# Optimization experiments

Hardware: AMD Instinct MI355X
Metric: run time of the kernel (lower is better)

The kernel has to match this reference:

```python
import jax, jax.numpy as jnp
import numpy as np

NUM_FILTER = 256
CAPS_LEN = 8
NUM_EMOTIONS = 8
OUT_DIM = 16
NUM_CHANNEL = 25
TIME_LEN = 25
NUM_CAPS = NUM_CHANNEL * TIME_LEN * (NUM_FILTER // CAPS_LEN)  # 20000
NUM_ITERATIONS = 3


def setup_inputs() -> dict:
    key = jax.random.key(0)
    ks = jax.random.split(key, 10)
    B = 32
    x = jax.random.normal(ks[0], (B, 54, 54), jnp.float32)
    conv1_w = jax.random.normal(ks[1], (NUM_FILTER, 1, 6, 6), jnp.float32) * 0.05
    conv1_b = jax.random.normal(ks[2], (NUM_FILTER,), jnp.float32) * 0.01
    conv2_w = jax.random.normal(ks[3], (NUM_FILTER, NUM_FILTER, 6, 6), jnp.float32) * 0.01
    conv2_b = jax.random.normal(ks[4], (NUM_FILTER,), jnp.float32) * 0.01
    conv3_w = jax.random.normal(ks[5], (NUM_FILTER, 2 * NUM_FILTER, 1, 1), jnp.float32) * 0.05
    conv3_b = jax.random.normal(ks[6], (NUM_FILTER,), jnp.float32) * 0.01
    # PrimaryCaps: one Linear(caps_len -> caps_len) per capsule, batched as [nc, out, in]
    pc_w = jax.random.normal(ks[7], (NUM_CAPS, CAPS_LEN, CAPS_LEN), jnp.float32) * 0.1
    pc_b = jax.random.normal(ks[8], (NUM_CAPS, CAPS_LEN), jnp.float32) * 0.1
    # EmotionCaps transform W: [nc, num_emotions, out_dim, in_dim]
    W = jax.random.normal(ks[9], (NUM_CAPS, NUM_EMOTIONS, OUT_DIM, CAPS_LEN), jnp.float32) * 0.05
    return {"x": x, "conv1_w": conv1_w, "conv1_b": conv1_b, "conv2_w": conv2_w,
            "conv2_b": conv2_b, "conv3_w": conv3_w, "conv3_b": conv3_b,
            "pc_w": pc_w, "pc_b": pc_b, "W": W}


def _conv(x, w, b, stride):
    y = jax.lax.conv_general_dilated(x, w, (stride, stride), 'VALID',
                                     dimension_numbers=('NCHW', 'OIHW', 'NCHW'))
    return y + b[None, :, None, None]


def _squash(s):
    # scale = |s|^2 / (1 + |s|^2); out = scale * s / (|s| + 1e-8)
    n2 = jnp.sum(s * s, axis=-1, keepdims=True)
    n = jnp.sqrt(n2)
    return (n2 / (1.0 + n2)) * s / (n + 1e-8)


def reference(x, conv1_w, conv1_b, conv2_w, conv2_b, conv3_w, conv3_b, pc_w, pc_b, W):
    x4 = x[:, None]                                    # [B,1,54,54]
    x1 = jax.nn.relu(_conv(x4, conv1_w, conv1_b, 2))   # [B,F,25,25]
    y = jnp.pad(x1, ((0, 0), (0, 0), (2, 3), (2, 3)))  # ZeroPad2d((2,3,2,3))
    y = jax.nn.relu(_conv(y, conv2_w, conv2_b, 1))     # [B,F,25,25]
    z = jax.nn.relu(jnp.concatenate([x1, y], axis=1))  # [B,2F,25,25]
    z = _conv(z, conv3_w, conv3_b, 1)                  # [B,F,25,25]
    B, F, H, Wd = z.shape
    # flatten to capsules: [B, F//caps_len, caps_len, H*W] -> [B, nc, caps_len]
    caps = z.reshape(B, F // CAPS_LEN, CAPS_LEN, H * Wd)
    caps = caps.transpose(0, 1, 3, 2).reshape(B, NUM_CAPS, CAPS_LEN)
    # PrimaryCaps: per-capsule linear, batched as a single einsum
    u = jnp.einsum('bni,noi->bno', caps, pc_w) + pc_b[None]   # [B,nc,caps_len]
    # EmotionCaps: u_hat[b,n,e,o] = W[n,e,o,i] u[b,n,i]
    u_hat = jnp.einsum('bni,neoi->bneo', u, W)                # [B,nc,ne,out_dim]
    b = jnp.zeros((B, NUM_CAPS, NUM_EMOTIONS), u.dtype)
    v = None
    for r in range(NUM_ITERATIONS):
        c = jax.nn.softmax(b, axis=2)[..., None]              # [B,nc,ne,1]
        v = _squash(jnp.sum(c * u_hat, axis=1))               # [B,ne,out_dim]
        if r < NUM_ITERATIONS - 1:
            b = b + jnp.einsum('bneo,beo->bne', u_hat, v)
    return jnp.linalg.norm(v, axis=-1)                        # [B,ne]
```

## Files before the change

kernel.cpp:

```cpp
#include <hip/hip_runtime.h>

typedef unsigned short u16;
typedef __attribute__((ext_vector_type(8))) short bf16x8;
typedef __attribute__((ext_vector_type(4))) float floatx4;

#define NPIX 625
#define NCAPS 20000
#define K2 9216

__device__ __forceinline__ u16 f2bf(float f) {
  unsigned u = __float_as_uint(f);
  return (u16)((u + 0x7fffu + ((u >> 16) & 1u)) >> 16);
}

__device__ __forceinline__ float bf2f(unsigned v) {
  return __uint_as_float(v << 16);
}

#define GLDS16(g, l) __builtin_amdgcn_global_load_lds( \
    (const __attribute__((address_space(1))) void*)(g), \
    (__attribute__((address_space(3))) void*)(l), 16, 0, 0)

__global__ void prep_weights2(const float* __restrict__ w2, const float* __restrict__ w3,
                              u16* __restrict__ A2c, u16* __restrict__ A3) {
  if (blockIdx.x < 256) {
    const int oc = blockIdx.x, c = threadIdx.x;
    const float* src = w2 + (oc * 256 + c) * 36;
    float v[36];
#pragma unroll
    for (int k = 0; k < 9; k++) {
      const float4 q = *(const float4*)(src + k * 4);
      v[k * 4 + 0] = q.x; v[k * 4 + 1] = q.y; v[k * 4 + 2] = q.z; v[k * 4 + 3] = q.w;
    }
    const int mtile = oc >> 7, row = oc & 127;
#pragma unroll
    for (int t = 0; t < 36; t++) {
      const int kt = t / 9, tl = t % 9;
      A2c[(kt * 2 + mtile) * 294912 + row * 2304 + tl * 256 + c] = f2bf(v[t]);
    }
  } else {
    const int j = (blockIdx.x - 256) * 1024 + threadIdx.x * 4;
    const float4 q = *(const float4*)(w3 + j);
    ushort4 p;
    p.x = f2bf(q.x); p.y = f2bf(q.y); p.z = f2bf(q.z); p.w = f2bf(q.w);
    *(ushort4*)(A3 + j) = p;
  }
}

__global__ void prep_wbs(const float* __restrict__ W, u16* __restrict__ Wbs) {
  int r = blockIdx.x * 256 + threadIdx.x;
  int n = r >> 7, eo = r & 127;
  int e = eo >> 4, o = eo & 15;
  const float* src = W + n * 1024 + eo * 8;
  const float4 v0 = *(const float4*)src;
  const float4 v1 = *(const float4*)(src + 4);
  u16* dst = Wbs + n * 1088 + e * 136 + o * 8;
  ushort4 p0, p1;
  p0.x = f2bf(v0.x); p0.y = f2bf(v0.y); p0.z = f2bf(v0.z); p0.w = f2bf(v0.w);
  p1.x = f2bf(v1.x); p1.y = f2bf(v1.y); p1.z = f2bf(v1.z); p1.w = f2bf(v1.w);
  *(ushort4*)dst = p0;
  *(ushort4*)(dst + 4) = p1;
}

__global__ void conv1_kernel(const float* __restrict__ x, const float* __restrict__ w1,
                             const float* __restrict__ b1, u16* __restrict__ x1p) {
  int blk = blockIdx.x;
  int b = blk / 25, i = blk % 25;
  int f = threadIdx.x;
  float wreg[36];
#pragma unroll
  for (int k = 0; k < 36; k++) wreg[k] = w1[f * 36 + k];
  float bias = b1[f];
  const float* xb = x + b * 54 * 54 + (2 * i) * 54;
  for (int j = 0; j < 25; j++) {
    float acc = bias;
#pragma unroll
    for (int ki = 0; ki < 6; ki++)
#pragma unroll
      for (int kj = 0; kj < 6; kj++)
        acc = fmaf(xb[ki * 54 + 2 * j + kj], wreg[ki * 6 + kj], acc);
    x1p[(((b * 30 + i + 2) * 30) + (j + 2)) * 256 + f] = f2bf(fmaxf(acc, 0.f));
  }
}

__global__ __launch_bounds__(256) void conv2_gemm(const u16* __restrict__ A2c,
    const u16* __restrict__ x1p, u16* __restrict__ P) {
  __shared__ u16 As0[128 * 32];
  __shared__ u16 Bs0[128 * 32];
  __shared__ u16 As1[128 * 32];
  __shared__ u16 Bs1[128 * 32];
  const int tid = threadIdx.x;
  const int lane = tid & 63, wave = tid >> 6;
  const int f = blockIdx.x;
  const int w = (f & 7) * 157 + (f >> 3);
  const int ntile = w >> 3, combo = w & 7;
  const int kt = combo >> 1, mtile = combo & 1;
  const int t0 = kt * 9;

  const int seg0 = tid, seg1 = tid + 256;
  const u16* gA0 = A2c + combo * 294912 + (seg0 >> 2) * 2304 + (seg0 & 3) * 8;
  const u16* gA1 = A2c + combo * 294912 + (seg1 >> 2) * 2304 + (seg1 & 3) * 8;

  auto pixbase = [&](int seg) {
    int n = ntile * 128 + (seg >> 2);
    if (n > NCAPS - 1) n = NCAPS - 1;
    int b = n / NPIX, p = n % NPIX;
    int i = p / 25, j = p % 25;
    return ((b * 30 + i) * 30 + j) * 256 + (seg & 3) * 8;
  };
  const u16* gb0 = x1p + pixbase(seg0);
  const u16* gb1 = x1p + pixbase(seg1);

// ... 24 lines not shown
        bfr[tt] = *(const bf16x8*)(Bs0 + (wn * 64 + tt * 16 + lrow) * 32 + kgrp * 8);
      }
#pragma unroll
      for (int tm = 0; tm < 4; tm++)
#pragma unroll
        for (int tn = 0; tn < 4; tn++)
          acc[tm][tn] = __builtin_amdgcn_mfma_f32_16x16x32_bf16(af[tm], bfr[tn], acc[tm][tn], 0, 0, 0);
#pragma unroll
      for (int tt = 0; tt < 4; tt++) {
        af[tt]  = *(const bf16x8*)(As1 + (wm * 64 + tt * 16 + lrow) * 32 + kgrp * 8);
        bfr[tt] = *(const bf16x8*)(Bs1 + (wn * 64 + tt * 16 + lrow) * 32 + kgrp * 8);
      }
#pragma unroll
      for (int tm = 0; tm < 4; tm++)
#pragma unroll
        for (int tn = 0; tn < 4; tn++)
          acc[tm][tn] = __builtin_amdgcn_mfma_f32_16x16x32_bf16(af[tm], bfr[tn], acc[tm][tn], 0, 0, 0);
      __syncthreads();
    }
    boff += 256;
    kj++;
    if (kj == 6) { kj = 0; boff += 6144; }
  }

  u16* Pk = P + kt * 5120000;
  const int nb = ntile * 128 + wn * 64;
  const int ocb = mtile * 128 + wm * 64 + kgrp * 4;
#pragma unroll
  for (int tn = 0; tn < 4; tn++) {
    int n = nb + tn * 16 + lrow;
    if (n < NCAPS) {
#pragma unroll
      for (int tm = 0; tm < 4; tm++) {
        int oc = ocb + tm * 16;
        ushort4 pk;
        pk.x = f2bf(acc[tm][tn][0]);
        pk.y = f2bf(acc[tm][tn][1]);
        pk.z = f2bf(acc[tm][tn][2]);
        pk.w = f2bf(acc[tm][tn][3]);
        *(ushort4*)(Pk + n * 256 + oc) = pk;
      }
    }
  }
}

__global__ void conv2_red(const u16* __restrict__ P, const float* __restrict__ bias2,
                          u16* __restrict__ y) {
  const int idx = blockIdx.x * 256 + threadIdx.x;
  const ushort4 p0 = *(const ushort4*)(P + idx * 4);
  const ushort4 p1 = *(const ushort4*)(P + 5120000 + idx * 4);
  const ushort4 p2 = *(const ushort4*)(P + 10240000 + idx * 4);
  const ushort4 p3 = *(const ushort4*)(P + 15360000 + idx * 4);
  const float4 bs = *(const float4*)(bias2 + ((idx * 4) & 255));
  float sx = bf2f(p0.x) + bf2f(p1.x) + bf2f(p2.x) + bf2f(p3.x) + bs.x;
  float sy = bf2f(p0.y) + bf2f(p1.y) + bf2f(p2.y) + bf2f(p3.y) + bs.y;
  float sz = bf2f(p0.z) + bf2f(p1.z) + bf2f(p2.z) + bf2f(p3.z) + bs.z;
  float sw = bf2f(p0.w) + bf2f(p1.w) + bf2f(p2.w) + bf2f(p3.w) + bs.w;
  ushort4 pk;
  pk.x = f2bf(fmaxf(sx, 0.f));
  pk.y = f2bf(fmaxf(sy, 0.f));
  pk.z = f2bf(fmaxf(sz, 0.f));
  pk.w = f2bf(fmaxf(sw, 0.f));
  *(ushort4*)(y + idx * 4) = pk;
}

__global__ __launch_bounds__(256) void conv3_gemm(const u16* __restrict__ A3,
    const u16* __restrict__ x1p, const u16* __restrict__ y,
    const float* __restrict__ bias3, float* __restrict__ z) {
  __shared__ u16 As[128 * 32];
  __shared__ u16 Bs[128 * 32];
  const int tid = threadIdx.x;
  const int lane = tid & 63, wave = tid >> 6;
  const int mtile = blockIdx.x, ntile = blockIdx.y;

  const int seg0 = tid, seg1 = tid + 256;
  const u16* ga0 = A3 + (mtile * 128 + (seg0 >> 2)) * 512 + (seg0 & 3) * 8;
  const u16* ga1 = A3 + (mtile * 128 + (seg1 >> 2)) * 512 + (seg1 & 3) * 8;

  auto mkbases = [&](int seg, const u16*& gx, const u16*& gy) {
    int n = ntile * 128 + (seg >> 2);
    if (n > NCAPS - 1) n = NCAPS - 1;
    int b = n / NPIX, p = n % NPIX;
    int i = p / 25, j = p % 25;
    gx = x1p + ((b * 30 + i + 2) * 30 + (j + 2)) * 256 + (seg & 3) * 8;
    gy = y + n * 256 + (seg & 3) * 8;
  };
  const u16 *gx0, *gy0, *gx1, *gy1;
  mkbases(seg0, gx0, gy0);
  mkbases(seg1, gx1, gy1);

  floatx4 acc[4][4] = {};
  const int wm = wave & 1, wn = wave >> 1;
  const int lrow = lane & 15, kgrp = lane >> 4;

  for (int kc = 0; kc < 16; kc++) {
    const u16* s0 = (kc < 8) ? (gx0 + kc * 32) : (gy0 + (kc - 8) * 32);
    const u16* s1 = (kc < 8) ? (gx1 + kc * 32) : (gy1 + (kc - 8) * 32);
    GLDS16(ga0 + kc * 32, As + seg0 * 8);
    GLDS16(ga1 + kc * 32, As + seg1 * 8);
    GLDS16(s0, Bs + seg0 * 8);
    GLDS16(s1, Bs + seg1 * 8);
    __syncthreads();
    bf16x8 af[4], bfr[4];
#pragma unroll
    for (int tt = 0; tt < 4; tt++) {
      af[tt]  = *(const bf16x8*)(As + (wm * 64 + tt * 16 + lrow) * 32 + kgrp * 8);
      bfr[tt] = *(const bf16x8*)(Bs + (wn * 64 + tt * 16 + lrow) * 32 + kgrp * 8);
    }
#pragma unroll
    for (int tm = 0; tm < 4; tm++)
#pragma unroll
      for (int tn = 0; tn < 4; tn++)
        acc[tm][tn] = __builtin_amdgcn_mfma_f32_16x16x32_bf16(af[tm], bfr[tn], acc[tm][tn], 0, 0, 0);
    __syncthreads();
  }

  const int nb = ntile * 128 + wn * 64;
  const int fb = mtile * 128 + wm * 64 + kgrp * 4;
#pragma unroll
  for (int tn = 0; tn < 4; tn++) {
    int n = nb + tn * 16 + lrow;
    if (n < NCAPS) {
#pragma unroll
      for (int tm = 0; tm < 4; tm++) {
        int f0 = fb + tm * 16;
        float4 v;
        v.x = acc[tm][tn][0] + bias3[f0 + 0];
        v.y = acc[tm][tn][1] + bias3[f0 + 1];
        v.z = acc[tm][tn][2] + bias3[f0 + 2];
        v.w = acc[tm][tn][3] + bias3[f0 + 3];
        *(float4*)(z + n * 256 + f0) = v;
      }
    }
  }
}


__device__ __forceinline__ float dot8v(float4 a0, float4 a1, float4 b0, float4 b1) {
  float s = a0.x * b0.x;
  s = fmaf(a0.y, b0.y, s); s = fmaf(a0.z, b0.z, s); s = fmaf(a0.w, b0.w, s);
  s = fmaf(a1.x, b1.x, s); s = fmaf(a1.y, b1.y, s);
  s = fmaf(a1.z, b1.z, s); s = fmaf(a1.w, b1.w, s);
  return s;
}

__device__ __forceinline__ float dotrow(uint4 w, float4 ua, float4 ub) {
  float s = __uint_as_float(w.x << 16) * ua.x;
  s = fmaf(__uint_as_float(w.x & 0xffff0000u), ua.y, s);
  s = fmaf(__uint_as_float(w.y << 16), ua.z, s);
  s = fmaf(__uint_as_float(w.y & 0xffff0000u), ua.w, s);
  s = fmaf(__uint_as_float(w.z << 16), ub.x, s);
  s = fmaf(__uint_as_float(w.z & 0xffff0000u), ub.y, s);
  s = fmaf(__uint_as_float(w.w << 16), ub.z, s);
  s = fmaf(__uint_as_float(w.w & 0xffff0000u), ub.w, s);
  return s;
}

__global__ void caps_u(const float* __restrict__ z, const float* __restrict__ pcw,
                       const float* __restrict__ pcb, float* __restrict__ u) {
  const int tid = threadIdx.x;
  const int b = tid >> 3, o = tid & 7;
  for (int k = 0; k < 8; k++) {
    const int n = blockIdx.x * 8 + k;
    const int g = n / NPIX, p = n % NPIX;
    const float* zp = z + (b * NPIX + p) * 256 + g * 8;
    float4 c0 = *(const float4*)zp;
    float4 c1 = *(const float4*)(zp + 4);
    const float* pw = pcw + n * 64 + o * 8;
    float4 w0 = *(const float4*)pw;
    float4 w1 = *(const float4*)(pw + 4);
    u[n * 256 + tid] = pcb[n * 8 + o] + dot8v(w0, w1, c0, c1);
  }
}

__global__ void caps_u2(const float* __restrict__ z, const float* __restrict__ pcw,
                        const float* __restrict__ pcb, unsigned* __restrict__ u2) {
  const int tid = threadIdx.x;
  const int b = tid >> 3, o = tid & 7;
  for (int k = 0; k < 8; k++) {
    const int n = blockIdx.x * 8 + k;
    const int g = n / NPIX, p = n % NPIX;
    const float* zp = z + (b * NPIX + p) * 256 + g * 8;
    float4 c0 = *(const float4*)zp;
    float4 c1 = *(const float4*)(zp + 4);
    const float* pw = pcw + n * 64 + o * 8;
    float4 w0 = *(const float4*)pw;
    float4 w1 = *(const float4*)(pw + 4);
    const float myu = pcb[n * 8 + o] + dot8v(w0, w1, c0, c1);
    const float partner = __shfl_xor(myu, 1, 64);
    if (!(o & 1)) {
      unsigned pk = (unsigned)f2bf(myu) | ((unsigned)f2bf(partner) << 16);
      u2[n * 128 + b * 4 + (o >> 1)] = pk;
    }
  }
}

__global__ __launch_bounds__(256, 4) void caps_accb2(const unsigned* __restrict__ u2,
    const u16* __restrict__ Wbs, const float* __restrict__ vsum,
    float* __restrict__ Spart) {
  __shared__ u16 Ws[16 * 1088];
  const int tid = threadIdx.x;
  const int b = tid >> 3, e = tid & 7;
  const int n0 = blockIdx.x * 16;

  const u16* gsrc = Wbs + n0 * 1088;
#pragma unroll
  for (int k = 0; k < 9; k++) {
    const int idx = k * 256 + tid;
    if (idx < 2176) GLDS16(gsrc + idx * 8, Ws + idx * 8);
  }

  const float* vp = vsum + tid * 16;
  const float4 V0 = *(const float4*)vp;
  const float4 V1 = *(const float4*)(vp + 4);
  const float4 V2 = *(const float4*)(vp + 8);
  const float4 V3 = *(const float4*)(vp + 12);
  float s0 = 0.f, s1 = 0.f, s2 = 0.f, s3 = 0.f, s4 = 0.f, s5 = 0.f, s6 = 0.f, s7 = 0.f;
  float s8 = 0.f, s9 = 0.f, s10 = 0.f, s11 = 0.f, s12 = 0.f, s13 = 0.f, s14 = 0.f, s15 = 0.f;

  __syncthreads();

  for (int it = 0; it < 16; it++) {
    const int n = n0 + it;
    const uint4 up = *(const uint4*)(u2 + n * 128 + b * 4);
    float4 ua, ub;
    ua.x = __uint_as_float(up.x << 16); ua.y = __uint_as_float(up.x & 0xffff0000u);
    ua.z = __uint_as_float(up.y << 16); ua.w = __uint_as_float(up.y & 0xffff0000u);
    ub.x = __uint_as_float(up.z << 16); ub.y = __uint_as_float(up.z & 0xffff0000u);
    ub.z = __uint_as_float(up.w << 16); ub.w = __uint_as_float(up.w & 0xffff0000u);

    const u16* Wn = Ws + it * 1088 + e * 136;
    float h0, h1, h2, h3, h4, h5, h6, h7, h8, h9, h10, h11, h12, h13, h14, h15;
#define ROW(o, H) { uint4 w = *(const uint4*)(Wn + (o) * 8); H = dotrow(w, ua, ub); }
    ROW(0, h0)   ROW(1, h1)   ROW(2, h2)   ROW(3, h3)
    ROW(4, h4)   ROW(5, h5)   ROW(6, h6)   ROW(7, h7)
    ROW(8, h8)   ROW(9, h9)   ROW(10, h10) ROW(11, h11)
    ROW(12, h12) ROW(13, h13) ROW(14, h14) ROW(15, h15)
#undef ROW
    float blog = h0 * V0.x;
    blog = fmaf(h1, V0.y, blog);  blog = fmaf(h2, V0.z, blog);  blog = fmaf(h3, V0.w, blog);
    blog = fmaf(h4, V1.x, blog);  blog = fmaf(h5, V1.y, blog);  blog = fmaf(h6, V1.z, blog);
    blog = fmaf(h7, V1.w, blog);  blog = fmaf(h8, V2.x, blog);  blog = fmaf(h9, V2.y, blog);
    blog = fmaf(h10, V2.z, blog); blog = fmaf(h11, V2.w, blog); blog = fmaf(h12, V3.x, blog);
    blog = fmaf(h13, V3.y, blog); blog = fmaf(h14, V3.z, blog); blog = fmaf(h15, V3.w, blog);
    float m = blog;
    m = fmaxf(m, __shfl_xor(m, 1, 64));
    m = fmaxf(m, __shfl_xor(m, 2, 64));
    m = fmaxf(m, __shfl_xor(m, 4, 64));
    float ex = __expf(blog - m);
    float ss = ex;
    ss += __shfl_xor(ss, 1, 64);
    ss += __shfl_xor(ss, 2, 64);
    ss += __shfl_xor(ss, 4, 64);
    const float c = ex / ss;
    s0 = fmaf(c, h0, s0);   s1 = fmaf(c, h1, s1);   s2 = fmaf(c, h2, s2);   s3 = fmaf(c, h3, s3);
    s4 = fmaf(c, h4, s4);   s5 = fmaf(c, h5, s5);   s6 = fmaf(c, h6, s6);   s7 = fmaf(c, h7, s7);
    s8 = fmaf(c, h8, s8);   s9 = fmaf(c, h9, s9);   s10 = fmaf(c, h10, s10); s11 = fmaf(c, h11, s11);
    s12 = fmaf(c, h12, s12); s13 = fmaf(c, h13, s13); s14 = fmaf(c, h14, s14); s15 = fmaf(c, h15, s15);
  }
  float* Sp = Spart + blockIdx.x * 4096 + tid * 16;
  *(float4*)(Sp + 0)  = make_float4(s0, s1, s2, s3);
  *(float4*)(Sp + 4)  = make_float4(s4, s5, s6, s7);
  *(float4*)(Sp + 8)  = make_float4(s8, s9, s10, s11);
  *(float4*)(Sp + 12) = make_float4(s12, s13, s14, s15);
}

__global__ __launch_bounds__(256, 2) void caps_acc(const float* __restrict__ u,
    const float* __restrict__ W, const float* __restrict__ vsum,
    float* __restrict__ Spart) {
  const int tid = threadIdx.x;
  const int b = tid >> 3, e = tid & 7;
  const float* vp = vsum + tid * 16;
  const float4 V0 = *(const float4*)vp;
  const float4 V1 = *(const float4*)(vp + 4);
  const float4 V2 = *(const float4*)(vp + 8);
  const float4 V3 = *(const float4*)(vp + 12);
  float s0 = 0.f, s1 = 0.f, s2 = 0.f, s3 = 0.f, s4 = 0.f, s5 = 0.f, s6 = 0.f, s7 = 0.f;
  float s8 = 0.f, s9 = 0.f, s10 = 0.f, s11 = 0.f, s12 = 0.f, s13 = 0.f, s14 = 0.f, s15 = 0.f;
  const int n0 = blockIdx.x * 16;
  for (int it = 0; it < 16; it++) {
    const int n = n0 + it;
    const float* un = u + n * 256 + (b << 3);
    const float4 u0 = *(const float4*)un;
    const float4 u1 = *(const float4*)(un + 4);
    const float* Wn = W + n * 1024 + e * 128;
    float h0, h1, h2, h3, h4, h5, h6, h7, h8, h9, h10, h11, h12, h13, h14, h15;
#define OST(o, H) { float4 wa = *(const float4*)(Wn + (o) * 8); \
                    float4 wb = *(const float4*)(Wn + (o) * 8 + 4); \
                    H = dot8v(wa, wb, u0, u1); }
    OST(0, h0)  OST(1, h1)  OST(2, h2)  OST(3, h3)
    OST(4, h4)  OST(5, h5)  OST(6, h6)  OST(7, h7)
    OST(8, h8)  OST(9, h9)  OST(10, h10) OST(11, h11)
    OST(12, h12) OST(13, h13) OST(14, h14) OST(15, h15)
#undef OST
    float blog = h0 * V0.x;
    blog = fmaf(h1, V0.y, blog);  blog = fmaf(h2, V0.z, blog);  blog = fmaf(h3, V0.w, blog);
    blog = fmaf(h4, V1.x, blog);  blog = fmaf(h5, V1.y, blog);  blog = fmaf(h6, V1.z, blog);
    blog = fmaf(h7, V1.w, blog);  blog = fmaf(h8, V2.x, blog);  blog = fmaf(h9, V2.y, blog);
    blog = fmaf(h10, V2.z, blog); blog = fmaf(h11, V2.w, blog); blog = fmaf(h12, V3.x, blog);
    blog = fmaf(h13, V3.y, blog); blog = fmaf(h14, V3.z, blog); blog = fmaf(h15, V3.w, blog);
    float m = blog;
    m = fmaxf(m, __shfl_xor(m, 1, 64));
    m = fmaxf(m, __shfl_xor(m, 2, 64));
    m = fmaxf(m, __shfl_xor(m, 4, 64));
    float ex = __expf(blog - m);
    float ss = ex;
    ss += __shfl_xor(ss, 1, 64);
    ss += __shfl_xor(ss, 2, 64);
    ss += __shfl_xor(ss, 4, 64);
    const float c = ex / ss;
    s0 = fmaf(c, h0, s0);   s1 = fmaf(c, h1, s1);   s2 = fmaf(c, h2, s2);   s3 = fmaf(c, h3, s3);
    s4 = fmaf(c, h4, s4);   s5 = fmaf(c, h5, s5);   s6 = fmaf(c, h6, s6);   s7 = fmaf(c, h7, s7);
    s8 = fmaf(c, h8, s8);   s9 = fmaf(c, h9, s9);   s10 = fmaf(c, h10, s10); s11 = fmaf(c, h11, s11);
    s12 = fmaf(c, h12, s12); s13 = fmaf(c, h13, s13); s14 = fmaf(c, h14, s14); s15 = fmaf(c, h15, s15);
  }
  float* Sp = Spart + blockIdx.x * 4096 + tid * 16;
  *(float4*)(Sp + 0)  = make_float4(s0, s1, s2, s3);
  *(float4*)(Sp + 4)  = make_float4(s4, s5, s6, s7);
  *(float4*)(Sp + 8)  = make_float4(s8, s9, s10, s11);
  *(float4*)(Sp + 12) = make_float4(s12, s13, s14, s15);
}

__global__ void caps_redB(const float* __restrict__ Spart, float* __restrict__ Sp2) {
  const int j = blockIdx.x * 256 + threadIdx.x;
  const int r0 = blockIdx.y * 50;
  float a0 = 0.f, a1 = 0.f;
  for (int r = 0; r < 50; r += 2) {
    a0 += Spart[(r0 + r) * 4096 + j];
    a1 += Spart[(r0 + r + 1) * 4096 + j];
  }
  Sp2[blockIdx.y * 4096 + j] = a0 + a1;
}

__global__ void caps_v2(const float* __restrict__ Sp2, float* __restrict__ vsum, int add) {
  const int t = threadIdx.x;
  float4 a0 = make_float4(0.f, 0.f, 0.f, 0.f), a1 = a0, a2 = a0, a3 = a0;
  for (int r = 0; r < 25; r++) {
    const float* sp = Sp2 + r * 4096 + t * 16;
    const float4 q0 = *(const float4*)sp;
    const float4 q1 = *(const float4*)(sp + 4);
    const float4 q2 = *(const float4*)(sp + 8);
    const float4 q3 = *(const float4*)(sp + 12);
    a0.x += q0.x; a0.y += q0.y; a0.z += q0.z; a0.w += q0.w;
    a1.x += q1.x; a1.y += q1.y; a1.z += q1.z; a1.w += q1.w;
    a2.x += q2.x; a2.y += q2.y; a2.z += q2.z; a2.w += q2.w;
    a3.x += q3.x; a3.y += q3.y; a3.z += q3.z; a3.w += q3.w;
  }
  float n2 = a0.x * a0.x;
  n2 = fmaf(a0.y, a0.y, n2); n2 = fmaf(a0.z, a0.z, n2); n2 = fmaf(a0.w, a0.w, n2);
  n2 = fmaf(a1.x, a1.x, n2); n2 = fmaf(a1.y, a1.y, n2); n2 = fmaf(a1.z, a1.z, n2); n2 = fmaf(a1.w, a1.w, n2);
  n2 = fmaf(a2.x, a2.x, n2); n2 = fmaf(a2.y, a2.y, n2); n2 = fmaf(a2.z, a2.z, n2); n2 = fmaf(a2.w, a2.w, n2);
  n2 = fmaf(a3.x, a3.x, n2); n2 = fmaf(a3.y, a3.y, n2); n2 = fmaf(a3.z, a3.z, n2); n2 = fmaf(a3.w, a3.w, n2);
  const float n = sqrtf(n2);
  const float scale = n2 / ((1.f + n2) * (n + 1e-8f));
  float* vp = vsum + t * 16;
  float4 o0, o1, o2, o3;
  if (add) {
    o0 = *(float4*)(vp + 0); o1 = *(float4*)(vp + 4); o2 = *(float4*)(vp + 8); o3 = *(float4*)(vp + 12);
  } else {
    o0 = make_float4(0.f, 0.f, 0.f, 0.f); o1 = o0; o2 = o0; o3 = o0;
  }
  o0.x = fmaf(a0.x, scale, o0.x); o0.y = fmaf(a0.y, scale, o0.y);
  o0.z = fmaf(a0.z, scale, o0.z); o0.w = fmaf(a0.w, scale, o0.w);
  o1.x = fmaf(a1.x, scale, o1.x); o1.y = fmaf(a1.y, scale, o1.y);
  o1.z = fmaf(a1.z, scale, o1.z); o1.w = fmaf(a1.w, scale, o1.w);
  o2.x = fmaf(a2.x, scale, o2.x); o2.y = fmaf(a2.y, scale, o2.y);
  o2.z = fmaf(a2.z, scale, o2.z); o2.w = fmaf(a2.w, scale, o2.w);
  o3.x = fmaf(a3.x, scale, o3.x); o3.y = fmaf(a3.y, scale, o3.y);
  o3.z = fmaf(a3.z, scale, o3.z); o3.w = fmaf(a3.w, scale, o3.w);
  *(float4*)(vp + 0) = o0; *(float4*)(vp + 4) = o1;
  *(float4*)(vp + 8) = o2; *(float4*)(vp + 12) = o3;
}

__global__ void caps_out2(const float* __restrict__ Sp2, float* __restrict__ out) {
  const int t = threadIdx.x;
  float4 a0 = make_float4(0.f, 0.f, 0.f, 0.f), a1 = a0, a2 = a0, a3 = a0;
  for (int r = 0; r < 25; r++) {
    const float* sp = Sp2 + r * 4096 + t * 16;
    const float4 q0 = *(const float4*)sp;
    const float4 q1 = *(const float4*)(sp + 4);
    const float4 q2 = *(const float4*)(sp + 8);
    const float4 q3 = *(const float4*)(sp + 12);
    a0.x += q0.x; a0.y += q0.y; a0.z += q0.z; a0.w += q0.w;
    a1.x += q1.x; a1.y += q1.y; a1.z += q1.z; a1.w += q1.w;
    a2.x += q2.x; a2.y += q2.y; a2.z += q2.z; a2.w += q2.w;
    a3.x += q3.x; a3.y += q3.y; a3.z += q3.z; a3.w += q3.w;
  }
  float n2 = a0.x * a0.x;
  n2 = fmaf(a0.y, a0.y, n2); n2 = fmaf(a0.z, a0.z, n2); n2 = fmaf(a0.w, a0.w, n2);
  n2 = fmaf(a1.x, a1.x, n2); n2 = fmaf(a1.y, a1.y, n2); n2 = fmaf(a1.z, a1.z, n2); n2 = fmaf(a1.w, a1.w, n2);
  n2 = fmaf(a2.x, a2.x, n2); n2 = fmaf(a2.y, a2.y, n2); n2 = fmaf(a2.z, a2.z, n2); n2 = fmaf(a2.w, a2.w, n2);
  n2 = fmaf(a3.x, a3.x, n2); n2 = fmaf(a3.y, a3.y, n2); n2 = fmaf(a3.z, a3.z, n2); n2 = fmaf(a3.w, a3.w, n2);
  const float n = sqrtf(n2);
  out[t] = n * n2 / ((1.f + n2) * (n + 1e-8f));
}

__global__ void caps_redA(const float* __restrict__ Spart, float* __restrict__ S) {
  const int j = blockIdx.x * 256 + threadIdx.x;
  const int r0 = blockIdx.y * 50;
  float a0 = 0.f, a1 = 0.f;
  for (int r = 0; r < 50; r += 2) {
    a0 += Spart[(r0 + r) * 4096 + j];
    a1 += Spart[(r0 + r + 1) * 4096 + j];
  }
  atomicAdd(&S[j], a0 + a1);
}

__global__ void caps_v(const float* __restrict__ S, float* __restrict__ vsum, int add) {
  const int t = threadIdx.x;
  const float* sp = S + t * 16;
  const float4 a0 = *(const float4*)sp;
  const float4 a1 = *(const float4*)(sp + 4);
  const float4 a2 = *(const float4*)(sp + 8);
  const float4 a3 = *(const float4*)(sp + 12);
  float n2 = a0.x * a0.x;
  n2 = fmaf(a0.y, a0.y, n2); n2 = fmaf(a0.z, a0.z, n2); n2 = fmaf(a0.w, a0.w, n2);
  n2 = fmaf(a1.x, a1.x, n2); n2 = fmaf(a1.y, a1.y, n2); n2 = fmaf(a1.z, a1.z, n2); n2 = fmaf(a1.w, a1.w, n2);
  n2 = fmaf(a2.x, a2.x, n2); n2 = fmaf(a2.y, a2.y, n2); n2 = fmaf(a2.z, a2.z, n2); n2 = fmaf(a2.w, a2.w, n2);
  n2 = fmaf(a3.x, a3.x, n2); n2 = fmaf(a3.y, a3.y, n2); n2 = fmaf(a3.z, a3.z, n2); n2 = fmaf(a3.w, a3.w, n2);
  const float n = sqrtf(n2);
  const float scale = n2 / ((1.f + n2) * (n + 1e-8f));
  float* vp = vsum + t * 16;
  float4 o0, o1, o2, o3;
  if (add) {
    o0 = *(float4*)(vp + 0); o1 = *(float4*)(vp + 4); o2 = *(float4*)(vp + 8); o3 = *(float4*)(vp + 12);
  } else {
    o0 = make_float4(0.f, 0.f, 0.f, 0.f); o1 = o0; o2 = o0; o3 = o0;
  }
  o0.x = fmaf(a0.x, scale, o0.x); o0.y = fmaf(a0.y, scale, o0.y);
  o0.z = fmaf(a0.z, scale, o0.z); o0.w = fmaf(a0.w, scale, o0.w);
  o1.x = fmaf(a1.x, scale, o1.x); o1.y = fmaf(a1.y, scale, o1.y);
  o1.z = fmaf(a1.z, scale, o1.z); o1.w = fmaf(a1.w, scale, o1.w);
  o2.x = fmaf(a2.x, scale, o2.x); o2.y = fmaf(a2.y, scale, o2.y);
  o2.z = fmaf(a2.z, scale, o2.z); o2.w = fmaf(a2.w, scale, o2.w);
  o3.x = fmaf(a3.x, scale, o3.x); o3.y = fmaf(a3.y, scale, o3.y);
  o3.z = fmaf(a3.z, scale, o3.z); o3.w = fmaf(a3.w, scale, o3.w);
  *(float4*)(vp + 0) = o0; *(float4*)(vp + 4) = o1;
  *(float4*)(vp + 8) = o2; *(float4*)(vp + 12) = o3;
}

__global__ void caps_out(const float* __restrict__ S, float* __restrict__ out) {
  const int t = threadIdx.x;
  const float* sp = S + t * 16;
  const float4 a0 = *(const float4*)sp;
  const float4 a1 = *(const float4*)(sp + 4);
  const float4 a2 = *(const float4*)(sp + 8);
  const float4 a3 = *(const float4*)(sp + 12);
  float n2 = a0.x * a0.x;
  n2 = fmaf(a0.y, a0.y, n2); n2 = fmaf(a0.z, a0.z, n2); n2 = fmaf(a0.w, a0.w, n2);
  n2 = fmaf(a1.x, a1.x, n2); n2 = fmaf(a1.y, a1.y, n2); n2 = fmaf(a1.z, a1.z, n2); n2 = fmaf(a1.w, a1.w, n2);
  n2 = fmaf(a2.x, a2.x, n2); n2 = fmaf(a2.y, a2.y, n2); n2 = fmaf(a2.z, a2.z, n2); n2 = fmaf(a2.w, a2.w, n2);
  n2 = fmaf(a3.x, a3.x, n2); n2 = fmaf(a3.y, a3.y, n2); n2 = fmaf(a3.z, a3.z, n2); n2 = fmaf(a3.w, a3.w, n2);
  const float n = sqrtf(n2);
  out[t] = n * n2 / ((1.f + n2) * (n + 1e-8f));
}

extern "C" void kernel_launch(void* const* d_in, const int* in_sizes, int n_in,
                              void* d_out, int out_size, void* d_ws, size_t ws_size,
                              hipStream_t stream) {
  const float* x   = (const float*)d_in[0];
  const float* w1  = (const float*)d_in[1];
  const float* b1  = (const float*)d_in[2];
  const float* w2  = (const float*)d_in[3];
  const float* b2  = (const float*)d_in[4];
  const float* w3  = (const float*)d_in[5];
  const float* b3  = (const float*)d_in[6];
  const float* pcw = (const float*)d_in[7];
  const float* pcb = (const float*)d_in[8];
  const float* W   = (const float*)d_in[9];
  float* out = (float*)d_out;

  char* ws = (char*)d_ws;
  const bool use_bf16w = (ws_size >= (size_t)75000000);

  u16*   x1p = (u16*)(ws + 0);
  u16*   A2  = (u16*)(ws + 14745600);
  u16*   A3  = (u16*)(ws + 19464192);
  u16*   y   = (u16*)(ws + 19726336);
  u16*   P   = (u16*)(ws + 29966336);

  u16* Wbs;
  unsigned* u2;
  float *z, *Spart, *u, *S, *vs, *Sp2;
  if (use_bf16w) {
    Wbs   = (u16*)(ws + 0);
    z     = (float*)(ws + 43520000);
    Spart = (float*)(ws + 43520000);
    u2    = (unsigned*)(ws + 64000000);
    Sp2   = (float*)(ws + 74240000);
    vs    = (float*)(ws + 74649600);
    u = nullptr; S = nullptr;
  } else {
    Wbs = nullptr; u2 = nullptr; Sp2 = nullptr;
    z     = (float*)(ws + 29966336);
    Spart = (float*)(ws + 29966336);
    u     = (float*)(ws + 50446336);
    S     = (float*)(ws + 70926336);
    vs    = (float*)(ws + 70942720);
  }

  hipMemsetAsync(x1p, 0, 14745600, stream);
  hipMemsetAsync(vs, 0, 16384, stream);

  prep_weights2<<<384, 256, 0, stream>>>(w2, w3, A2, A3);
  conv1_kernel<<<800, 256, 0, stream>>>(x, w1, b1, x1p);
  conv2_gemm<<<1256, 256, 0, stream>>>(A2, x1p, P);
  conv2_red<<<5000, 256, 0, stream>>>(P, b2, y);
  conv3_gemm<<<dim3(2, 157), 256, 0, stream>>>(A3, x1p, y, b3, z);
  if (use_bf16w) {
    prep_wbs<<<10000, 256, 0, stream>>>(W, Wbs);
    caps_u2<<<2500, 256, 0, stream>>>(z, pcw, pcb, u2);
  } else {
    caps_u<<<2500, 256, 0, stream>>>(z, pcw, pcb, u);
  }

  for (int pass = 0; pass < 3; pass++) {
    if (use_bf16w) {
      caps_accb2<<<1250, 256, 0, stream>>>(u2, Wbs, vs, Spart);
      caps_redB<<<dim3(16, 25), 256, 0, stream>>>(Spart, Sp2);
      if (pass == 0)      caps_v2<<<1, 256, 0, stream>>>(Sp2, vs, 0);
      else if (pass == 1) caps_v2<<<1, 256, 0, stream>>>(Sp2, vs, 1);
      else                caps_out2<<<1, 256, 0, stream>>>(Sp2, out);
    } else {
      caps_acc<<<1250, 256, 0, stream>>>(u, W, vs, Spart);
      hipMemsetAsync(S, 0, 16384, stream);
      caps_redA<<<dim3(16, 25), 256, 0, stream>>>(Spart, S);
      if (pass == 0)      caps_v<<<1, 256, 0, stream>>>(S, vs, 0);
      else if (pass == 1) caps_v<<<1, 256, 0, stream>>>(S, vs, 1);
      else                caps_out<<<1, 256, 0, stream>>>(S, out);
    }
  }
}
```

Before: 503.8 us.

## Split-K conv3 with bf16 partials and fp16 dot2 capsule transform

Conv3 GEMM is split across two K-halves (x1 and y sources) via a third grid dimension, each writing bf16 partial outputs that caps_u2 sums along with the bias, replacing the fp32 z buffer. The capsule weights W and u vectors are now stored as fp16 instead of bf16, so the per-row dot products use packed fp16 dot2 instructions instead of unpacking to fp32 FMAs. The fallback fp32 path is removed. This doubles conv3 block count and halves intermediate traffic, at the cost of extra rounding in the bf16 partials and the fp16 range and precision limits.

New measurement: 454.1 us. -9.9%, faster.

```diff
diff --git a/kernel.cpp b/kernel.cpp
--- a/kernel.cpp
+++ b/kernel.cpp
@@ -1,8 +1,10 @@
 #include <hip/hip_runtime.h>
+#include <hip/hip_fp16.h>
 
 typedef unsigned short u16;
 typedef __attribute__((ext_vector_type(8))) short bf16x8;
 typedef __attribute__((ext_vector_type(4))) float floatx4;
+typedef __attribute__((ext_vector_type(2))) _Float16 half2v;
 
 #define NPIX 625
 #define NCAPS 20000
@@ -13,8 +15,41 @@
   return (u16)((u + 0x7fffu + ((u >> 16) & 1u)) >> 16);
 }
 
-__device__ __forceinline__ float bf2f(unsigned v) {
-  return __uint_as_float(v << 16);
+__device__ __forceinline__ unsigned h16(float f) {
+  union { _Float16 h; u16 b; } c;
+  c.h = (_Float16)f;
+  return (unsigned)c.b;
+}
+
+__device__ __forceinline__ half2v as_h2(unsigned u) {
+  union { unsigned i; half2v h; } c;
+  c.i = u;
+  return c.h;
+}
+
+__device__ __forceinline__ float dot2f(unsigned a, unsigned b, float c) {
+#if __has_builtin(__builtin_amdgcn_fdot2)
+  return __builtin_amdgcn_fdot2(as_h2(a), as_h2(b), c, false);
+#else
+  half2v x = as_h2(a), y = as_h2(b);
+  return fmaf((float)x[1], (float)y[1], fmaf((float)x[0], (float)y[0], c));
+#endif
+}
+
+__device__ __forceinline__ float dotrow16(uint4 w, uint4 u) {
+  float s = dot2f(w.x, u.x, 0.f);
+  s = dot2f(w.y, u.y, s);
+  s = dot2f(w.z, u.z, s);
+  s = dot2f(w.w, u.w, s);
+  return s;
+}
+
+__device__ __forceinline__ float dot8v(float4 a0, float4 a1, float4 b0, float4 b1) {
+  float s = a0.x * b0.x;
+  s = fmaf(a0.y, b0.y, s); s = fmaf(a0.z, b0.z, s); s = fmaf(a0.w, b0.w, s);
+  s = fmaf(a1.x, b1.x, s); s = fmaf(a1.y, b1.y, s);
+  s = fmaf(a1.z, b1.z, s); s = fmaf(a1.w, b1.w, s);
+  return s;
 }
 
 #define GLDS16(g, l) __builtin_amdgcn_global_load_lds( \
@@ -56,8 +91,8 @@
   const float4 v1 = *(const float4*)(src + 4);
   u16* dst = Wbs + n * 1088 + e * 136 + o * 8;
   ushort4 p0, p1;
-  p0.x = f2bf(v0.x); p0.y = f2bf(v0.y); p0.z = f2bf(v0.z); p0.w = f2bf(v0.w);
-  p1.x = f2bf(v1.x); p1.y = f2bf(v1.y); p1.z = f2bf(v1.z); p1.w = f2bf(v1.w);
+  p0.x = (u16)h16(v0.x); p0.y = (u16)h16(v0.y); p0.z = (u16)h16(v0.z); p0.w = (u16)h16(v0.w);
+  p1.x = (u16)h16(v1.x); p1.y = (u16)h16(v1.y); p1.z = (u16)h16(v1.z); p1.w = (u16)h16(v1.w);
   *(ushort4*)dst = p0;
   *(ushort4*)(dst + 4) = p1;
 }
@@ -188,10 +223,11 @@
   const ushort4 p2 = *(const ushort4*)(P + 10240000 + idx * 4);
   const ushort4 p3 = *(const ushort4*)(P + 15360000 + idx * 4);
   const float4 bs = *(const float4*)(bias2 + ((idx * 4) & 255));
-  float sx = bf2f(p0.x) + bf2f(p1.x) + bf2f(p2.x) + bf2f(p3.x) + bs.x;
-  float sy = bf2f(p0.y) + bf2f(p1.y) + bf2f(p2.y) + bf2f(p3.y) + bs.y;
-  float sz = bf2f(p0.z) + bf2f(p1.z) + bf2f(p2.z) + bf2f(p3.z) + bs.z;
-  float sw = bf2f(p0.w) + bf2f(p1.w) + bf2f(p2.w) + bf2f(p3.w) + bs.w;
+  auto bf = [](unsigned v) { return __uint_as_float(v << 16); };
+  float sx = bf(p0.x) + bf(p1.x) + bf(p2.x) + bf(p3.x) + bs.x;
+  float sy = bf(p0.y) + bf(p1.y) + bf(p2.y) + bf(p3.y) + bs.y;
+  float sz = bf(p0.z) + bf(p1.z) + bf(p2.z) + bf(p3.z) + bs.z;
+  float sw = bf(p0.w) + bf(p1.w) + bf(p2.w) + bf(p3.w) + bs.w;
   ushort4 pk;
   pk.x = f2bf(fmaxf(sx, 0.f));
   pk.y = f2bf(fmaxf(sy, 0.f));
@@ -201,41 +237,39 @@
 }
 
 __global__ __launch_bounds__(256) void conv3_gemm(const u16* __restrict__ A3,
-    const u16* __restrict__ x1p, const u16* __restrict__ y,
-    const float* __restrict__ bias3, float* __restrict__ z) {
+    const u16* __restrict__ x1p, const u16* __restrict__ y, u16* __restrict__ P3) {
   __shared__ u16 As[128 * 32];
   __shared__ u16 Bs[128 * 32];
   const int tid = threadIdx.x;
   const int lane = tid & 63, wave = tid >> 6;
-  const int mtile = blockIdx.x, ntile = blockIdx.y;
+  const int mtile = blockIdx.x, ntile = blockIdx.y, kt = blockIdx.z;
 
   const int seg0 = tid, seg1 = tid + 256;
-  const u16* ga0 = A3 + (mtile * 128 + (seg0 >> 2)) * 512 + (seg0 & 3) * 8;
-  const u16* ga1 = A3 + (mtile * 128 + (seg1 >> 2)) * 512 + (seg1 & 3) * 8;
-
-  auto mkbases = [&](int seg, const u16*& gx, const u16*& gy) {
+  const u16* ga0 = A3 + (mtile * 128 + (seg0 >> 2)) * 512 + (seg0 & 3) * 8 + kt * 256;
+  const u16* ga1 = A3 + (mtile * 128 + (seg1 >> 2)) * 512 + (seg1 & 3) * 8 + kt * 256;
+
+  auto mkbase = [&](int seg) {
     int n = ntile * 128 + (seg >> 2);
     if (n > NCAPS - 1) n = NCAPS - 1;
-    int b = n / NPIX, p = n % NPIX;
-    int i = p / 25, j = p % 25;
-    gx = x1p + ((b * 30 + i + 2) * 30 + (j + 2)) * 256 + (seg & 3) * 8;
-    gy = y + n * 256 + (seg & 3) * 8;
+    if (kt == 0) {
+      int b = n / NPIX, p = n % NPIX;
+      int i = p / 25, j = p % 25;
+      return x1p + ((b * 30 + i + 2) * 30 + (j + 2)) * 256 + (seg & 3) * 8;
+    }
+    return y + n * 256 + (seg & 3) * 8;
   };
-  const u16 *gx0, *gy0, *gx1, *gy1;
-  mkbases(seg0, gx0, gy0);
-  mkbases(seg1, gx1, gy1);
+  const u16* gs0 = mkbase(seg0);
+  const u16* gs1 = mkbase(seg1);
 
   floatx4 acc[4][4] = {};
   const int wm = wave & 1, wn = wave >> 1;
   const int lrow = lane & 15, kgrp = lane >> 4;
 
-  for (int kc = 0; kc < 16; kc++) {
-    const u16* s0 = (kc < 8) ? (gx0 + kc * 32) : (gy0 + (kc - 8) * 32);
-    const u16* s1 = (kc < 8) ? (gx1 + kc * 32) : (gy1 + (kc - 8) * 32);
+  for (int kc = 0; kc < 8; kc++) {
     GLDS16(ga0 + kc * 32, As + seg0 * 8);
     GLDS16(ga1 + kc * 32, As + seg1 * 8);
-    GLDS16(s0, Bs + seg0 * 8);
-    GLDS16(s1, Bs + seg1 * 8);
+    GLDS16(gs0 + kc * 32, Bs + seg0 * 8);
+    GLDS16(gs1 + kc * 32, Bs + seg1 * 8);
     __syncthreads();
     bf16x8 af[4], bfr[4];
 #pragma unroll
@@ -251,6 +285,7 @@
     __syncthreads();
   }
 
+  u16* Pk = P3 + kt * 5120000;
   const int nb = ntile * 128 + wn * 64;
   const int fb = mtile * 128 + wm * 64 + kgrp * 4;
 #pragma unroll
@@ -260,72 +295,48 @@
 #pragma unroll
       for (int tm = 0; tm < 4; tm++) {
         int f0 = fb + tm * 16;
-        float4 v;
-        v.x = acc[tm][tn][0] + bias3[f0 + 0];
-        v.y = acc[tm][tn][1] + bias3[f0 + 1];
-        v.z = acc[tm][tn][2] + bias3[f0 + 2];
-        v.w = acc[tm][tn][3] + bias3[f0 + 3];
-        *(float4*)(z + n * 256 + f0) = v;
+        ushort4 pk;
+        pk.x = f2bf(acc[tm][tn][0]);
+        pk.y = f2bf(acc[tm][tn][1]);
+        pk.z = f2bf(acc[tm][tn][2]);
+        pk.w = f2bf(acc[tm][tn][3]);
+        *(ushort4*)(Pk + n * 256 + f0) = pk;
       }
     }
   }
 }
 
 
-__device__ __forceinline__ float dot8v(float4 a0, float4 a1, float4 b0, float4 b1) {
-  float s = a0.x * b0.x;
-  s = fmaf(a0.y, b0.y, s); s = fmaf(a0.z, b0.z, s); s = fmaf(a0.w, b0.w, s);
-  s = fmaf(a1.x, b1.x, s); s = fmaf(a1.y, b1.y, s);
-  s = fmaf(a1.z, b1.z, s); s = fmaf(a1.w, b1.w, s);
-  return s;
-}
-
-__device__ __forceinline__ float dotrow(uint4 w, float4 ua, float4 ub) {
-  float s = __uint_as_float(w.x << 16) * ua.x;
-  s = fmaf(__uint_as_float(w.x & 0xffff0000u), ua.y, s);
-  s = fmaf(__uint_as_float(w.y << 16), ua.z, s);
-  s = fmaf(__uint_as_float(w.y & 0xffff0000u), ua.w, s);
-  s = fmaf(__uint_as_float(w.z << 16), ub.x, s);
-  s = fmaf(__uint_as_float(w.z & 0xffff0000u), ub.y, s);
-  s = fmaf(__uint_as_float(w.w << 16), ub.z, s);
-  s = fmaf(__uint_as_float(w.w & 0xffff0000u), ub.w, s);
-  return s;
-}
-
-__global__ void caps_u(const float* __restrict__ z, const float* __restrict__ pcw,
-                       const float* __restrict__ pcb, float* __restrict__ u) {
+__global__ void caps_u2(const u16* __restrict__ P3, const float* __restrict__ b3,
+                        const float* __restrict__ pcw, const float* __restrict__ pcb,
+                        unsigned* __restrict__ u2) {
   const int tid = threadIdx.x;
   const int b = tid >> 3, o = tid & 7;
   for (int k = 0; k < 8; k++) {
     const int n = blockIdx.x * 8 + k;
     const int g = n / NPIX, p = n % NPIX;
-    const float* zp = z + (b * NPIX + p) * 256 + g * 8;
-    float4 c0 = *(const float4*)zp;
-    float4 c1 = *(const float4*)(zp + 4);
-    const float* pw = pcw + n * 64 + o * 8;
-    float4 w0 = *(const float4*)pw;
-    float4 w1 = *(const float4*)(pw + 4);
-    u[n * 256 + tid] = pcb[n * 8 + o] + dot8v(w0, w1, c0, c1);
-  }
-}
-
-__global__ void caps_u2(const float* __restrict__ z, const float* __restrict__ pcw,
-                        const float* __restrict__ pcb, unsigned* __restrict__ u2) {
-  const int tid = threadIdx.x;
-  const int b = tid >> 3, o = tid & 7;
-  for (int k = 0; k < 8; k++) {
-    const int n = blockIdx.x * 8 + k;
-    const int g = n / NPIX, p = n % NPIX;
-    const float* zp = z + (b * NPIX + p) * 256 + g * 8;
-    float4 c0 = *(const float4*)zp;
-    float4 c1 = *(const float4*)(zp + 4);
+    const u16* pa = P3 + ((b * NPIX + p) * 256 + g * 8);
+    const uint4 qa = *(const uint4*)pa;
+    const uint4 qb = *(const uint4*)(pa + 5120000);
+    const float* bp = b3 + g * 8;
+    const float4 bb0 = *(const float4*)bp;
+    const float4 bb1 = *(const float4*)(bp + 4);
+    float4 c0, c1;
+    c0.x = __uint_as_float(qa.x << 16) + __uint_as_float(qb.x << 16) + bb0.x;
+    c0.y = __uint_as_float(qa.x & 0xffff0000u) + __uint_as_float(qb.x & 0xffff0000u) + bb0.y;
+    c0.z = __uint_as_float(qa.y << 16) + __uint_as_float(qb.y << 16) + bb0.z;
+    c0.w = __uint_as_float(qa.y & 0xffff0000u) + __uint_as_float(qb.y & 0xffff0000u) + bb0.w;
+    c1.x = __uint_as_float(qa.z << 16) + __uint_as_float(qb.z << 16) + bb1.x;
+    c1.y = __uint_as_float(qa.z & 0xffff0000u) + __uint_as_float(qb.z & 0xffff0000u) + bb1.y;
+    c1.z = __uint_as_float(qa.w << 16) + __uint_as_float(qb.w << 16) + bb1.z;
+    c1.w = __uint_as_float(qa.w & 0xffff0000u) + __uint_as_float(qb.w & 0xffff0000u) + bb1.w;
     const float* pw = pcw + n * 64 + o * 8;
     float4 w0 = *(const float4*)pw;
     float4 w1 = *(const float4*)(pw + 4);
     const float myu = pcb[n * 8 + o] + dot8v(w0, w1, c0, c1);
     const float partner = __shfl_xor(myu, 1, 64);
     if (!(o & 1)) {
-      unsigned pk = (unsigned)f2bf(myu) | ((unsigned)f2bf(partner) << 16);
+      unsigned pk = h16(myu) | (h16(partner) << 16);
       u2[n * 128 + b * 4 + (o >> 1)] = pk;
     }
   }
@@ -359,15 +370,9 @@
   for (int it = 0; it < 16; it++) {
     const int n = n0 + it;
     const uint4 up = *(const uint4*)(u2 + n * 128 + b * 4);
-    float4 ua, ub;
-    ua.x = __uint_as_float(up.x << 16); ua.y = __uint_as_float(up.x & 0xffff0000u);
-    ua.z = __uint_as_float(up.y << 16); ua.w = __uint_as_float(up.y & 0xffff0000u);
-    ub.x = __uint_as_float(up.z << 16); ub.y = __uint_as_float(up.z & 0xffff0000u);
-    ub.z = __uint_as_float(up.w << 16); ub.w = __uint_as_float(up.w & 0xffff0000u);
-
     const u16* Wn = Ws + it * 1088 + e * 136;
     float h0, h1, h2, h3, h4, h5, h6, h7, h8, h9, h10, h11, h12, h13, h14, h15;
-#define ROW(o, H) { uint4 w = *(const uint4*)(Wn + (o) * 8); H = dotrow(w, ua, ub); }
+#define ROW(o, H) { uint4 w = *(const uint4*)(Wn + (o) * 8); H = dotrow16(w, up); }
     ROW(0, h0)   ROW(1, h1)   ROW(2, h2)   ROW(3, h3)
     ROW(4, h4)   ROW(5, h5)   ROW(6, h6)   ROW(7, h7)
     ROW(8, h8)   ROW(9, h9)   ROW(10, h10) ROW(11, h11)
@@ -401,62 +406,6 @@
   *(float4*)(Sp + 12) = make_float4(s12, s13, s14, s15);
 }
 
-__global__ __launch_bounds__(256, 2) void caps_acc(const float* __restrict__ u,
-    const float* __restrict__ W, const float* __restrict__ vsum,
-    float* __restrict__ Spart) {
-  const int tid = threadIdx.x;
-  const int b = tid >> 3, e = tid & 7;
-  const float* vp = vsum + tid * 16;
-  const float4 V0 = *(const float4*)vp;
-  const float4 V1 = *(const float4*)(vp + 4);
-  const float4 V2 = *(const float4*)(vp + 8);
-  const float4 V3 = *(const float4*)(vp + 12);
-  float s0 = 0.f, s1 = 0.f, s2 = 0.f, s3 = 0.f, s4 = 0.f, s5 = 0.f, s6 = 0.f, s7 = 0.f;
-  float s8 = 0.f, s9 = 0.f, s10 = 0.f, s11 = 0.f, s12 = 0.f, s13 = 0.f, s14 = 0.f, s15 = 0.f;
-  const int n0 = blockIdx.x * 16;
-  for (int it = 0; it < 16; it++) {
-    const int n = n0 + it;
-    const float* un = u + n * 256 + (b << 3);
-    const float4 u0 = *(const float4*)un;
-    const float4 u1 = *(const float4*)(un + 4);
-    const float* Wn = W + n * 1024 + e * 128;
-    float h0, h1, h2, h3, h4, h5, h6, h7, h8, h9, h10, h11, h12, h13, h14, h15;
-#define OST(o, H) { float4 wa = *(const float4*)(Wn + (o) * 8); \
-                    float4 wb = *(const float4*)(Wn + (o) * 8 + 4); \
-                    H = dot8v(wa, wb, u0, u1); }
-    OST(0, h0)  OST(1, h1)  OST(2, h2)  OST(3, h3)
-    OST(4, h4)  OST(5, h5)  OST(6, h6)  OST(7, h7)
-    OST(8, h8)  OST(9, h9)  OST(10, h10) OST(11, h11)
-    OST(12, h12) OST(13, h13) OST(14, h14) OST(15, h15)
-#undef OST
-    float blog = h0 * V0.x;
-    blog = fmaf(h1, V0.y, blog);  blog = fmaf(h2, V0.z, blog);  blog = fmaf(h3, V0.w, blog);
-    blog = fmaf(h4, V1.x, blog);  blog = fmaf(h5, V1.y, blog);  blog = fmaf(h6, V1.z, blog);
-    blog = fmaf(h7, V1.w, blog);  blog = fmaf(h8, V2.x, blog);  blog = fmaf(h9, V2.y, blog);
-    blog = fmaf(h10, V2.z, blog); blog = fmaf(h11, V2.w, blog); blog = fmaf(h12, V3.x, blog);
-    blog = fmaf(h13, V3.y, blog); blog = fmaf(h14, V3.z, blog); blog = fmaf(h15, V3.w, blog);
-    float m = blog;
-    m = fmaxf(m, __shfl_xor(m, 1, 64));
-    m = fmaxf(m, __shfl_xor(m, 2, 64));
-    m = fmaxf(m, __shfl_xor(m, 4, 64));
-    float ex = __expf(blog - m);
-    float ss = ex;
-    ss += __shfl_xor(ss, 1, 64);
-    ss += __shfl_xor(ss, 2, 64);
-    ss += __shfl_xor(ss, 4, 64);
-    const float c = ex / ss;
-    s0 = fmaf(c, h0, s0);   s1 = fmaf(c, h1, s1);   s2 = fmaf(c, h2, s2);   s3 = fmaf(c, h3, s3);
-    s4 = fmaf(c, h4, s4);   s5 = fmaf(c, h5, s5);   s6 = fmaf(c, h6, s6);   s7 = fmaf(c, h7, s7);
-    s8 = fmaf(c, h8, s8);   s9 = fmaf(c, h9, s9);   s10 = fmaf(c, h10, s10); s11 = fmaf(c, h11, s11);
-    s12 = fmaf(c, h12, s12); s13 = fmaf(c, h13, s13); s14 = fmaf(c, h14, s14); s15 = fmaf(c, h15, s15);
-  }
-  float* Sp = Spart + blockIdx.x * 4096 + tid * 16;
-  *(float4*)(Sp + 0)  = make_float4(s0, s1, s2, s3);
-  *(float4*)(Sp + 4)  = make_float4(s4, s5, s6, s7);
-  *(float4*)(Sp + 8)  = make_float4(s8, s9, s10, s11);
-  *(float4*)(Sp + 12) = make_float4(s12, s13, s14, s15);
-}
-
 __global__ void caps_redB(const float* __restrict__ Spart, float* __restrict__ Sp2) {
   const int j = blockIdx.x * 256 + threadIdx.x;
   const int r0 = blockIdx.y * 50;
@@ -522,66 +471,6 @@
     a2.x += q2.x; a2.y += q2.y; a2.z += q2.z; a2.w += q2.w;
     a3.x += q3.x; a3.y += q3.y; a3.z += q3.z; a3.w += q3.w;
   }
-  float n2 = a0.x * a0.x;
-  n2 = fmaf(a0.y, a0.y, n2); n2 = fmaf(a0.z, a0.z, n2); n2 = fmaf(a0.w, a0.w, n2);
-  n2 = fmaf(a1.x, a1.x, n2); n2 = fmaf(a1.y, a1.y, n2); n2 = fmaf(a1.z, a1.z, n2); n2 = fmaf(a1.w, a1.w, n2);
-  n2 = fmaf(a2.x, a2.x, n2); n2 = fmaf(a2.y, a2.y, n2); n2 = fmaf(a2.z, a2.z, n2); n2 = fmaf(a2.w, a2.w, n2);
-  n2 = fmaf(a3.x, a3.x, n2); n2 = fmaf(a3.y, a3.y, n2); n2 = fmaf(a3.z, a3.z, n2); n2 = fmaf(a3.w, a3.w, n2);
-  const float n = sqrtf(n2);
-  out[t] = n * n2 / ((1.f + n2) * (n + 1e-8f));
-}
-
-__global__ void caps_redA(const float* __restrict__ Spart, float* __restrict__ S) {
-  const int j = blockIdx.x * 256 + threadIdx.x;
-  const int r0 = blockIdx.y * 50;
-  float a0 = 0.f, a1 = 0.f;
-  for (int r = 0; r < 50; r += 2) {
-    a0 += Spart[(r0 + r) * 4096 + j];
-    a1 += Spart[(r0 + r + 1) * 4096 + j];
-  }
-  atomicAdd(&S[j], a0 + a1);
-}
-
-__global__ void caps_v(const float* __restrict__ S, float* __restrict__ vsum, int add) {
-  const int t = threadIdx.x;
-  const float* sp = S + t * 16;
-  const float4 a0 = *(const float4*)sp;
-  const float4 a1 = *(const float4*)(sp + 4);
-  const float4 a2 = *(const float4*)(sp + 8);
-  const float4 a3 = *(const float4*)(sp + 12);
-  float n2 = a0.x * a0.x;
-  n2 = fmaf(a0.y, a0.y, n2); n2 = fmaf(a0.z, a0.z, n2); n2 = fmaf(a0.w, a0.w, n2);
-  n2 = fmaf(a1.x, a1.x, n2); n2 = fmaf(a1.y, a1.y, n2); n2 = fmaf(a1.z, a1.z, n2); n2 = fmaf(a1.w, a1.w, n2);
-  n2 = fmaf(a2.x, a2.x, n2); n2 = fmaf(a2.y, a2.y, n2); n2 = fmaf(a2.z, a2.z, n2); n2 = fmaf(a2.w, a2.w, n2);
-  n2 = fmaf(a3.x, a3.x, n2); n2 = fmaf(a3.y, a3.y, n2); n2 = fmaf(a3.z, a3.z, n2); n2 = fmaf(a3.w, a3.w, n2);
-  const float n = sqrtf(n2);
-  const float scale = n2 / ((1.f + n2) * (n + 1e-8f));
-  float* vp = vsum + t * 16;
-  float4 o0, o1, o2, o3;
-  if (add) {
-    o0 = *(float4*)(vp + 0); o1 = *(float4*)(vp + 4); o2 = *(float4*)(vp + 8); o3 = *(float4*)(vp + 12);
-  } else {
-    o0 = make_float4(0.f, 0.f, 0.f, 0.f); o1 = o0; o2 = o0; o3 = o0;
-  }
-  o0.x = fmaf(a0.x, scale, o0.x); o0.y = fmaf(a0.y, scale, o0.y);
-  o0.z = fmaf(a0.z, scale, o0.z); o0.w = fmaf(a0.w, scale, o0.w);
-  o1.x = fmaf(a1.x, scale, o1.x); o1.y = fmaf(a1.y, scale, o1.y);
-  o1.z = fmaf(a1.z, scale, o1.z); o1.w = fmaf(a1.w, scale, o1.w);
-  o2.x = fmaf(a2.x, scale, o2.x); o2.y = fmaf(a2.y, scale, o2.y);
-  o2.z = fmaf(a2.z, scale, o2.z); o2.w = fmaf(a2.w, scale, o2.w);
-  o3.x = fmaf(a3.x, scale, o3.x); o3.y = fmaf(a3.y, scale, o3.y);
-  o3.z = fmaf(a3.z, scale, o3.z); o3.w = fmaf(a3.w, scale, o3.w);
-  *(float4*)(vp + 0) = o0; *(float4*)(vp + 4) = o1;
-  *(float4*)(vp + 8) = o2; *(float4*)(vp + 12) = o3;
-}
-
-__global__ void caps_out(const float* __restrict__ S, float* __restrict__ out) {
-  const int t = threadIdx.x;
-  const float* sp = S + t * 16;
-  const float4 a0 = *(const float4*)sp;
-  const float4 a1 = *(const float4*)(sp + 4);
-  const float4 a2 = *(const float4*)(sp + 8);
-  const float4 a3 = *(const float4*)(sp + 12);
   float n2 = a0.x * a0.x;
   n2 = fmaf(a0.y, a0.y, n2); n2 = fmaf(a0.z, a0.z, n2); n2 = fmaf(a0.w, a0.w, n2);
   n2 = fmaf(a1.x, a1.x, n2); n2 = fmaf(a1.y, a1.y, n2); n2 = fmaf(a1.z, a1.z, n2); n2 = fmaf(a1.w, a1.w, n2);
@@ -607,33 +496,18 @@
   float* out = (float*)d_out;
 
   char* ws = (char*)d_ws;
-  const bool use_bf16w = (ws_size >= (size_t)75000000);
 
   u16*   x1p = (u16*)(ws + 0);
   u16*   A2  = (u16*)(ws + 14745600);
   u16*   A3  = (u16*)(ws + 19464192);
   u16*   y   = (u16*)(ws + 19726336);
   u16*   P   = (u16*)(ws + 29966336);
-
-  u16* Wbs;
-  unsigned* u2;
-  float *z, *Spart, *u, *S, *vs, *Sp2;
-  if (use_bf16w) {
-    Wbs   = (u16*)(ws + 0);
-    z     = (float*)(ws + 43520000);
-    Spart = (float*)(ws + 43520000);
-    u2    = (unsigned*)(ws + 64000000);
-    Sp2   = (float*)(ws + 74240000);
-    vs    = (float*)(ws + 74649600);
-    u = nullptr; S = nullptr;
-  } else {
-    Wbs = nullptr; u2 = nullptr; Sp2 = nullptr;
-    z     = (float*)(ws + 29966336);
-    Spart = (float*)(ws + 29966336);
-    u     = (float*)(ws + 50446336);
-    S     = (float*)(ws + 70926336);
-    vs    = (float*)(ws + 70942720);
-  }
+  u16*   P3  = (u16*)(ws + 43520000);
+  u16*   Wbs = (u16*)(ws + 0);
+  float* Spart = (float*)(ws + 43520000);
+  unsigned* u2 = (unsigned*)(ws + 64000000);
+  float* Sp2 = (float*)(ws + 74240000);
+  float* vs  = (float*)(ws + 74649600);
 
   hipMemsetAsync(x1p, 0, 14745600, stream);
   hipMemsetAsync(vs, 0, 16384, stream);
@@ -642,28 +516,15 @@
   conv1_kernel<<<800, 256, 0, stream>>>(x, w1, b1, x1p);
   conv2_gemm<<<1256, 256, 0, stream>>>(A2, x1p, P);
   conv2_red<<<5000, 256, 0, stream>>>(P, b2, y);
-  conv3_gemm<<<dim3(2, 157), 256, 0, stream>>>(A3, x1p, y, b3, z);
-  if (use_bf16w) {
-    prep_wbs<<<10000, 256, 0, stream>>>(W, Wbs);
-    caps_u2<<<2500, 256, 0, stream>>>(z, pcw, pcb, u2);
-  } else {
-    caps_u<<<2500, 256, 0, stream>>>(z, pcw, pcb, u);
-  }
+  conv3_gemm<<<dim3(2, 157, 2), 256, 0, stream>>>(A3, x1p, y, P3);
+  prep_wbs<<<10000, 256, 0, stream>>>(W, Wbs);
+  caps_u2<<<2500, 256, 0, stream>>>(P3, b3, pcw, pcb, u2);
 
   for (int pass = 0; pass < 3; pass++) {
-    if (use_bf16w) {
-      caps_accb2<<<1250, 256, 0, stream>>>(u2, Wbs, vs, Spart);
-      caps_redB<<<dim3(16, 25), 256, 0, stream>>>(Spart, Sp2);
-      if (pass == 0)      caps_v2<<<1, 256, 0, stream>>>(Sp2, vs, 0);
-      else if (pass == 1) caps_v2<<<1, 256, 0, stream>>>(Sp2, vs, 1);
-      else                caps_out2<<<1, 256, 0, stream>>>(Sp2, out);
-    } else {
-      caps_acc<<<1250, 256, 0, stream>>>(u, W, vs, Spart);
-      hipMemsetAsync(S, 0, 16384, stream);
-      caps_redA<<<dim3(16, 25), 256, 0, stream>>>(Spart, S);
-      if (pass == 0)      caps_v<<<1, 256, 0, stream>>>(S, vs, 0);
-      else if (pass == 1) caps_v<<<1, 256, 0, stream>>>(S, vs, 1);
-      else                caps_out<<<1, 256, 0, stream>>>(S, out);
-    }
-  }
-}
+    caps_accb2<<<1250, 256, 0, stream>>>(u2, Wbs, vs, Spart);
+    caps_redB<<<dim3(16, 25), 256, 0, stream>>>(Spart, Sp2);
+    if (pass == 0)      caps_v2<<<1, 256, 0, stream>>>(Sp2, vs, 0);
+    else if (pass == 1) caps_v2<<<1, 256, 0, stream>>>(Sp2, vs, 1);
+    else                caps_out2<<<1, 256, 0, stream>>>(Sp2, out);
+  }
+}
```
